# Optimization experiments

Hardware: AMD Instinct MI355X
Metric: run time of the kernel (lower is better)

Reference implementation:

```python
import jax, jax.numpy as jnp
import numpy as np

B, S_SRC, S_TGT, H, V = 32, 128, 64, 300, 32000


def setup_inputs() -> dict:
    key = jax.random.key(0)
    ks = jax.random.split(key, 16)

    def n(k, shape, scale=0.05):
        return jax.random.normal(k, shape, dtype=jnp.float32) * scale

    return {
        "x": jax.random.randint(ks[0], (B, S_SRC), 0, V),
        "y": jax.random.randint(ks[1], (B, S_TGT), 0, V),
        "h0": jax.random.normal(ks[2], (B, H), dtype=jnp.float32),  # encoder initNormState (L=1 squeezed)
        "EN": n(ks[3], (V, H)),
        "ZH": n(ks[4], (V, H)),
        "enc_Wih": n(ks[5], (H, H)),
        "enc_Whh": n(ks[6], (H, H)),
        "enc_bih": n(ks[7], (H,)),
        "enc_bhh": n(ks[8], (H,)),
        "dec_Wih": n(ks[9], (H, H)),
        "dec_Whh": n(ks[10], (H, H)),
        "dec_bih": n(ks[11], (H,)),
        "dec_bhh": n(ks[12], (H,)),
        "W_out": n(ks[13], (V, H)),
        "b_out": n(ks[14], (V,)),
    }


def reference(x, y, h0, EN, ZH, enc_Wih, enc_Whh, enc_bih, enc_bhh,
              dec_Wih, dec_Whh, dec_bih, dec_bhh, W_out, b_out):
    # ---- encoder: 1-layer tanh RNN over source embeddings ----
    xe = EN[x]  # [B, S_src, H]

    def enc_step(h, xt):  # xt: [B, H]
        h = jnp.tanh(xt @ enc_Wih.T + enc_bih + h @ enc_Whh.T + enc_bhh)
        return h, None

    c, _ = jax.lax.scan(enc_step, h0, jnp.swapaxes(xe, 0, 1))  # c: [B, H] final hidden

    # ---- decoder: original loop always feeds encoder state c (never the updated
    # hidden) to the RNNCell; with teacher forcing (start_TF_rate=1.0) every step
    # uses y_in[t], so all T steps vectorize into one batched computation. ----
    ye = ZH[y]  # [B, T, H]
    dec_state_term = c @ dec_Whh.T + dec_bhh  # [B, H], shared across all steps
    h_dec = jnp.tanh(ye @ dec_Wih.T + dec_bih + dec_state_term[:, None, :])  # [B, T, H]
    out = h_dec @ W_out.T + b_out  # [B, T, V]
    return out
```

## Files before the change

### kernel.cpp

```cpp
#include <hip/hip_runtime.h>
#include <hip/hip_bf16.h>
#include <stdint.h>

#define BB 32
#define S_SRC 128
#define S_TGT 64
#define H 300
#define VV 32000
#define M_ROWS (BB * S_TGT)
#define KP 320

#define MEGA_T 640
#define ENC_BLK 32
#define HDEC_BLK 128
#define WCVT_BLK 96

typedef __attribute__((ext_vector_type(8))) __bf16 bf16x8;
typedef __attribute__((ext_vector_type(4))) float f32x4;
typedef __attribute__((ext_vector_type(4))) unsigned short u16x4;
typedef __attribute__((ext_vector_type(2))) __fp16 f16x2;

#if defined(__has_builtin)
#if __has_builtin(__builtin_amdgcn_fdot2)
#define HAVE_FDOT2 1
#endif
#endif

__device__ inline unsigned short f2bf(float f) {
    union { float f; unsigned u; } v; v.f = f;
    unsigned r = (v.u + 0x7FFF + ((v.u >> 16) & 1)) >> 16;
    return (unsigned short)r;
}

__device__ __forceinline__ float ftanh(float x) {
    float e = __builtin_amdgcn_exp2f(x * 2.8853900817779268f);
    return 1.0f - 2.0f * __builtin_amdgcn_rcpf(e + 1.0f);
}

__device__ __forceinline__ float fdot2(f16x2 a, f16x2 b, float c) {
#ifdef HAVE_FDOT2
    return __builtin_amdgcn_fdot2(a, b, c, false);
#else
    return c + (float)a.x * (float)b.x + (float)a.y * (float)b.y;
#endif
}

__device__ __forceinline__ void gl_lds16(const void* g, void* l) {
    __builtin_amdgcn_global_load_lds(
        (const __attribute__((address_space(1))) void*)g,
        (__attribute__((address_space(3))) void*)l, 16, 0, 0);
}

__global__ void transpose2(const float* W0, const float* W1, float* dst) {
    const float* srcs[2] = {W0, W1};
    const float* src = srcs[blockIdx.z];
    float* d = dst + (size_t)blockIdx.z * (H * H);
    __shared__ float tile[32][33];
    int j0 = blockIdx.y * 32, k0 = blockIdx.x * 32;
    for (int r = threadIdx.y; r < 32; r += blockDim.y) {
        int j = j0 + r, k = k0 + threadIdx.x;
        tile[r][threadIdx.x] = (j < H && k < H) ? src[(size_t)j * H + k] : 0.f;
    }
    __syncthreads();
    for (int r = threadIdx.y; r < 32; r += blockDim.y) {
        int k = k0 + r, j = j0 + threadIdx.x;
        if (k < H && j < H) d[(size_t)k * H + j] = tile[threadIdx.x][r];
    }
}

#define RPB 8
__global__ __launch_bounds__(192) void pproj(const int* __restrict__ x,
                                             const float* __restrict__ EN,
                                             const float* __restrict__ WihT,
                                             const float* __restrict__ bih,
                                             const float* __restrict__ bhh,
                                             float* __restrict__ P) {
    __shared__ float xe[RPB][H];
    int m0 = blockIdx.x * RPB;
    int tid = threadIdx.x;
    for (int r = 0; r < RPB; ++r) {
        int idx = x[m0 + r];
        for (int c = tid; c < H; c += 192) xe[r][c] = EN[(size_t)idx * H + c];
    }
    __syncthreads();
    if (tid < 150) {
        int j = tid * 2;
        float a0[RPB], a1[RPB];
#pragma unroll
        for (int r = 0; r < RPB; ++r) { a0[r] = 0.f; a1[r] = 0.f; }
        const float* wp = WihT + j;
        for (int k = 0; k < H; ++k) {
            float2 w = *reinterpret_cast<const float2*>(wp + (size_t)k * H);
#pragma unroll
            for (int r = 0; r < RPB; ++r) {
                float xv = xe[r][k];
                a0[r] += xv * w.x; a1[r] += xv * w.y;
            }
        }
        float b0 = bih[j] + bhh[j], b1 = bih[j + 1] + bhh[j + 1];
#pragma unroll
        for (int r = 0; r < RPB; ++r) {
            P[(size_t)(m0 + r) * H + j]     = a0[r] + b0;
            P[(size_t)(m0 + r) * H + j + 1] = a1[r] + b1;
        }
    }
}

__global__ __launch_bounds__(MEGA_T) void mega(
    const float* __restrict__ h0, const float* __restrict__ P,
    const float* __restrict__ Whh,
    const float* __restrict__ dWhh, const float* __restrict__ dbhh,
    float* __restrict__ s2,
    const int* __restrict__ yv, const float* __restrict__ ZH,
    const float* __restrict__ WihT_d, const float* __restrict__ bih_d,
    float* __restrict__ t1,
    const float* __restrict__ W, unsigned short* __restrict__ Wb) {
    __shared__ union {
        __fp16 hb[2][304];
        float  ye[16][304];
    } L;
    int blk = blockIdx.x, tid = threadIdx.x;

    if (blk < ENC_BLK) {
        int b = blk;
        bool act = tid < 600;
        int j = tid >> 1, half = tid & 1;
        f16x2 w[76];
        if (act) {
            const float* wr = Whh + (size_t)j * H + half * 150;
#pragma unroll
            for (int i = 0; i < 75; ++i) {
                float2 f = *reinterpret_cast<const float2*>(wr + 2 * i);
                w[i] = __builtin_amdgcn_cvt_pkrtz(f.x, f.y);
            }
            w[75] = __builtin_amdgcn_cvt_pkrtz(0.f, 0.f);
        }
        if (act && half == 0) {
            int pos = j < 150 ? j : j + 2;
            L.hb[0][pos] = (__fp16)h0[(size_t)b * H + j];
        }
        if (tid >= 600 && tid < 608) {
            int pi = tid - 600, bufi = pi >> 2, q = pi & 3;
            int idx = (q < 2) ? (150 + q) : (302 + (q - 2));
            L.hb[bufi][idx] = (__fp16)0.f;
        }
        __syncthreads();

        const float* Pb = P + (size_t)b * S_SRC * H;
        int cur = 0;
        for (int t = 0; t < S_SRC; ++t) {
            float pv = 0.f;
            if (act && half == 0) pv = Pb[(size_t)t * H + j];
            if (act) {
                float a0 = 0.f, a1 = 0.f, a2 = 0.f, a3 = 0.f;
                const uint2* hp =
                    reinterpret_cast<const uint2*>(&L.hb[cur][half * 152]);
#pragma unroll
                for (int i = 0; i < 38; i += 2) {
                    uint2 qa = hp[i];
                    uint2 qb = hp[i + 1];
                    a0 = fdot2(w[2 * i],     __builtin_bit_cast(f16x2, qa.x), a0);
                    a1 = fdot2(w[2 * i + 1], __builtin_bit_cast(f16x2, qa.y), a1);
                    a2 = fdot2(w[2 * i + 2], __builtin_bit_cast(f16x2, qb.x), a2);
                    a3 = fdot2(w[2 * i + 3], __builtin_bit_cast(f16x2, qb.y), a3);
                }
                float a = (a0 + a1) + (a2 + a3);
                float tot = a + __shfl_xor(a, 1, 64);
                if (half == 0) {
                    float hv = ftanh(tot + pv);
                    int pos = j < 150 ? j : j + 2;
                    L.hb[cur ^ 1][pos] = (__fp16)hv;
                }
            }
            __syncthreads();
            cur ^= 1;
        }
        if (act) {
            const float* wr = dWhh + (size_t)j * H + half * 150;
            const uint2* hp = reinterpret_cast<const uint2*>(&L.hb[cur][half * 152]);
            float a0 = 0.f, a1 = 0.f;
#pragma unroll
            for (int i = 0; i < 37; ++i) {
                uint2 q = hp[i];
                f16x2 hA = __builtin_bit_cast(f16x2, q.x);
                f16x2 hB = __builtin_bit_cast(f16x2, q.y);
                float4 wf = *reinterpret_cast<const float4*>(wr + 4 * i);
                a0 += wf.x * (float)hA.x + wf.y * (float)hA.y;
                a1 += wf.z * (float)hB.x + wf.w * (float)hB.y;
            }
            {
                f16x2 hA = __builtin_bit_cast(f16x2,
                    reinterpret_cast<const uint*>(&L.hb[cur][half * 152])[74]);
                float2 wf = *reinterpret_cast<const float2*>(wr + 148);
                a0 += wf.x * (float)hA.x + wf.y * (float)hA.y;
            }
            float a = a0 + a1;
            float tot = a + __shfl_xor(a, 1, 64);
            if (half == 0) s2[(size_t)b * H + j] = tot + dbhh[j];
        }
    } else if (blk < ENC_BLK + HDEC_BLK) {
        int bi = blk - ENC_BLK;
        int m0 = bi * 16;
        for (int i = tid; i < 16 * 304; i += MEGA_T) {
            int r = i / 304, cc = i - r * 304;
            L.ye[r][cc] = (cc < H) ? ZH[(size_t)yv[m0 + r] * H + cc] : 0.f;
        }
        __syncthreads();
        if (tid < 600) {
            int rg = tid / 150, jp = tid - rg * 150, j0 = 2 * jp;
            float a[4][2] = {};
            const float* wp = WihT_d + j0;
            for (int k = 0; k < H; k += 2) {
                float2 wa = *reinterpret_cast<const float2*>(wp + (size_t)k * H);
                float2 wb = *reinterpret_cast<const float2*>(wp + (size_t)(k + 1) * H);
#pragma unroll
                for (int r = 0; r < 4; ++r) {
                    float2 x = *reinterpret_cast<const float2*>(&L.ye[rg * 4 + r][k]);
                    a[r][0] += x.x * wa.x + x.y * wb.x;
                    a[r][1] += x.x * wa.y + x.y * wb.y;
                }
            }
            float b0 = bih_d[j0], b1 = bih_d[j0 + 1];
#pragma unroll
            for (int r = 0; r < 4; ++r) {
                *reinterpret_cast<float2*>(&t1[(size_t)(m0 + rg * 4 + r) * 304 + j0]) =
                    make_float2(a[r][0] + b0, a[r][1] + b1);
            }
        }
    } else if (Wb != nullptr) {
        for (int id = (blk - (ENC_BLK + HDEC_BLK)) * MEGA_T + tid; id < VV * 80;
             id += WCVT_BLK * MEGA_T) {
            int row = id / 80, cq = id - row * 80;
            int k = cq * 4;
            u16x4 o;
            if (k < H) {
                float4 f = *reinterpret_cast<const float4*>(W + (size_t)row * H + k);
                o[0] = f2bf(f.x); o[1] = f2bf(f.y); o[2] = f2bf(f.z); o[3] = f2bf(f.w);
            } else {
                o[0] = 0; o[1] = 0; o[2] = 0; o[3] = 0;
            }
            *reinterpret_cast<u16x4*>(Wb + (size_t)row * KP + k) = o;
        }
    }
}

__global__ __launch_bounds__(256) void hdec_fin(const float* __restrict__ t1,
                                                const float* __restrict__ s2,
                                                unsigned short* __restrict__ hdec) {
    int blk = blockIdx.x, tid = threadIdx.x;
    for (int i = tid; i < 8 * KP; i += 256) {
        int r = i / KP, j = i - r * KP;
        int m = blk * 8 + r, b = m >> 6;
        unsigned short v = 0;
        if (j < H)
            v = f2bf(ftanh(t1[(size_t)m * 304 + j] + s2[(size_t)b * H + j]));
        hdec[(size_t)m * KP + j] = v;
    }
}

#define NBUF 4
__global__ __launch_bounds__(256, 2) void gemm4(const unsigned short* __restrict__ A,
                                                const unsigned short* __restrict__ Wb,
                                                const float* __restrict__ bout,
                                                float* __restrict__ out) {
    __shared__ unsigned short Al[NBUF][128 * 32];
    __shared__ unsigned short Bl[NBUF][128 * 32];
    int tid = threadIdx.x;
    int lane = tid & 63, wv = tid >> 6;
    int wm = wv >> 1, wn = wv & 1;

    int orig = blockIdx.x;
    int wg = (orig & 7) * 500 + (orig >> 3);
    int mi = wg & 15, ni = wg >> 4;
    int m0 = mi * 128, n0 = ni * 128;

    int rowq = tid >> 2;
    int scn = (tid & 3) ^ (rowq & 3);

    const unsigned short* Ab = A + (size_t)m0 * KP;
    const unsigned short* Bb = Wb + (size_t)n0 * KP;

    f32x4 acc[4][4];
    f32x4 zero = {0.f, 0.f, 0.f, 0.f};
#pragma unroll
    for (int i = 0; i < 4; ++i)
#pragma unroll
        for (int j = 0; j < 4; ++j) acc[i][j] = zero;

#define STAGE(T)                                                               \
    {                                                                          \
        int kk_ = (T) * 32;                                                    \
        int bf_ = (T) & 3;                                                     \
        _Pragma("unroll")                                                      \
        for (int s_ = 0; s_ < 2; ++s_) {                                       \
            int row_ = s_ * 64 + rowq;                                         \
            gl_lds16(Ab + (size_t)row_ * KP + kk_ + scn * 8,                   \
                     &Al[bf_][(s_ * 256 + tid) * 8]);                          \
        }                                                                      \
        _Pragma("unroll")                                                      \
        for (int s_ = 0; s_ < 2; ++s_) {                                       \
            int row_ = s_ * 64 + rowq;                                         \
            gl_lds16(Bb + (size_t)row_ * KP + kk_ + scn * 8,                   \
                     &Bl[bf_][(s_ * 256 + tid) * 8]);                          \
        }                                                                      \
    }

    STAGE(0) STAGE(1) STAGE(2)

#pragma unroll
    for (int t = 0; t < 10; ++t) {
        __builtin_amdgcn_sched_barrier(0);
        if (t < 8)       asm volatile("s_waitcnt vmcnt(8)" ::: "memory");
        else if (t == 8) asm volatile("s_waitcnt vmcnt(4)" ::: "memory");
        else             asm volatile("s_waitcnt vmcnt(0)" ::: "memory");
        __builtin_amdgcn_s_barrier();
        __builtin_amdgcn_sched_barrier(0);
        if (t + 3 < 10) STAGE(t + 3)
        int bf = t & 3;
        bf16x8 af[4], bb[4];
#pragma unroll
        for (int i = 0; i < 4; ++i) {
            int rowA = wm * 64 + i * 16 + (lane & 15);
            int chA = (lane >> 4) ^ (rowA & 3);
            af[i] = *reinterpret_cast<const bf16x8*>(&Al[bf][rowA * 32 + chA * 8]);
            int rowB = wn * 64 + i * 16 + (lane & 15);
            int chB = (lane >> 4) ^ (rowB & 3);
            bb[i] = *reinterpret_cast<const bf16x8*>(&Bl[bf][rowB * 32 + chB * 8]);
        }
        __builtin_amdgcn_s_setprio(1);
#pragma unroll
        for (int i = 0; i < 4; ++i)
#pragma unroll
            for (int j = 0; j < 4; ++j)
                acc[i][j] = __builtin_amdgcn_mfma_f32_16x16x32_bf16(
                    af[i], bb[j], acc[i][j], 0, 0, 0);
        __builtin_amdgcn_s_setprio(0);
    }
#undef STAGE

#pragma unroll
    for (int j = 0; j < 4; ++j) {
        int col = n0 + wn * 64 + j * 16 + (lane & 15);
        float bo = bout[col];
#pragma unroll
        for (int i = 0; i < 4; ++i) {
            int rb = m0 + wm * 64 + i * 16 + (lane >> 4) * 4;
            f32x4 v = acc[i][j];
#pragma unroll
            for (int r = 0; r < 4; ++r)
                out[(size_t)(rb + r) * VV + col] = v[r] + bo;
        }
    }
}

#define LDSW 40
__global__ __launch_bounds__(256) void gemm_out(const unsigned short* __restrict__ A,
                                                const float* __restrict__ W,
                                                const float* __restrict__ bout,
                                                float* __restrict__ out) {
    __shared__ __align__(16) unsigned short Alds[128 * LDSW];
    __shared__ __align__(16) unsigned short Bl[128 * LDSW];
    int tid = threadIdx.x;
    int lane = tid & 63, wv = tid >> 6;
    int wm = wv >> 1, wn = wv & 1;
    int m0 = blockIdx.y * 128, n0 = blockIdx.x * 128;

    f32x4 acc[4][4];
    f32x4 zero = {0.f, 0.f, 0.f, 0.f};
#pragma unroll
    for (int i = 0; i < 4; ++i)
#pragma unroll
        for (int jj = 0; jj < 4; ++jj) acc[i][jj] = zero;

    for (int k0 = 0; k0 < KP; k0 += 32) {
#pragma unroll
        for (int s = 0; s < 2; ++s) {
            int slot = tid + s * 256;
            int row = slot >> 2, c16 = slot & 3;
            uint4 v = *reinterpret_cast<const uint4*>(
                &A[(size_t)(m0 + row) * KP + k0 + c16 * 8]);
            *reinterpret_cast<uint4*>(&Alds[row * LDSW + c16 * 8]) = v;
        }
#pragma unroll
        for (int s = 0; s < 2; ++s) {
            int slot = tid + s * 256;
            int row = slot >> 2, c8 = slot & 3;
            int k = k0 + c8 * 8;
            __align__(16) unsigned short tmp[8];
            if (k + 7 < H) {
                const float* src = &W[(size_t)(n0 + row) * H + k];
                float4 f0 = *reinterpret_cast<const float4*>(src);
                float4 f1 = *reinterpret_cast<const float4*>(src + 4);
                tmp[0] = f2bf(f0.x); tmp[1] = f2bf(f0.y);
                tmp[2] = f2bf(f0.z); tmp[3] = f2bf(f0.w);
                tmp[4] = f2bf(f1.x); tmp[5] = f2bf(f1.y);
                tmp[6] = f2bf(f1.z); tmp[7] = f2bf(f1.w);
            } else {
#pragma unroll
                for (int jv = 0; jv < 8; ++jv) {
                    int kk = k + jv;
                    tmp[jv] = (kk < H) ? f2bf(W[(size_t)(n0 + row) * H + kk])
                                       : (unsigned short)0;
                }
            }
            *reinterpret_cast<uint4*>(&Bl[row * LDSW + c8 * 8]) =
                *reinterpret_cast<const uint4*>(tmp);
        }
        __syncthreads();
        bf16x8 af[4], bfm[4];
#pragma unroll
        for (int i = 0; i < 4; ++i) {
            int row = wm * 64 + i * 16 + (lane & 15);
            af[i] = *reinterpret_cast<const bf16x8*>(&Alds[row * LDSW + (lane >> 4) * 8]);
        }
#pragma unroll
        for (int i = 0; i < 4; ++i) {
            int row = wn * 64 + i * 16 + (lane & 15);
            bfm[i] = *reinterpret_cast<const bf16x8*>(&Bl[row * LDSW + (lane >> 4) * 8]);
        }
#pragma unroll
        for (int i = 0; i < 4; ++i)
#pragma unroll
            for (int jj = 0; jj < 4; ++jj)
                acc[i][jj] = __builtin_amdgcn_mfma_f32_16x16x32_bf16(
                    af[i], bfm[jj], acc[i][jj], 0, 0, 0);
        __syncthreads();
    }
#pragma unroll
    for (int jj = 0; jj < 4; ++jj) {
        int col = n0 + wn * 64 + jj * 16 + (lane & 15);
        float bo = bout[col];
#pragma unroll
        for (int i = 0; i < 4; ++i) {
            int rb = m0 + wm * 64 + i * 16 + (lane >> 4) * 4;
            f32x4 v = acc[i][jj];
#pragma unroll
            for (int r = 0; r < 4; ++r)
                out[(size_t)(rb + r) * VV + col] = v[r] + bo;
        }
    }
}

extern "C" void kernel_launch(void* const* d_in, const int* in_sizes, int n_in,
                              void* d_out, int out_size, void* d_ws, size_t ws_size,
                              hipStream_t stream) {
    const int*   x       = (const int*)d_in[0];
    const int*   y       = (const int*)d_in[1];
    const float* h0      = (const float*)d_in[2];
    const float* EN      = (const float*)d_in[3];
    const float* ZH      = (const float*)d_in[4];
    const float* enc_Wih = (const float*)d_in[5];
    const float* enc_Whh = (const float*)d_in[6];
    const float* enc_bih = (const float*)d_in[7];
    const float* enc_bhh = (const float*)d_in[8];
    const float* dec_Wih = (const float*)d_in[9];
    const float* dec_Whh = (const float*)d_in[10];
    const float* dec_bih = (const float*)d_in[11];
    const float* dec_bhh = (const float*)d_in[12];
    const float* W_out   = (const float*)d_in[13];
    const float* b_out   = (const float*)d_in[14];
    float* out = (float*)d_out;
    char* base = (char*)d_ws;

    const size_t needA = 22549120, needB = 2069120;
    bool bigws = (ws_size >= needA);
    if (!bigws && ws_size < needB) return;

    float* WT = (float*)base;
    float *s2_;
    unsigned short *hdec, *Wb = nullptr;
    if (bigws) {
        Wb   = (unsigned short*)(base + 720000);
        s2_  = (float*)(base + 21200000);
        hdec = (unsigned short*)(base + 21238400);
    } else {
        s2_  = (float*)(base + 720000);
        hdec = (unsigned short*)(base + 758400);
    }
    float* P  = out;
    float* t1 = out + 2000000;

    transpose2<<<dim3(10, 10, 2), dim3(32, 8), 0, stream>>>(enc_Wih, dec_Wih, WT);
    pproj<<<(BB * S_SRC) / RPB, 192, 0, stream>>>(x, EN, WT, enc_bih, enc_bhh, P);
    int mega_grid = bigws ? (ENC_BLK + HDEC_BLK + WCVT_BLK) : (ENC_BLK + HDEC_BLK);
    mega<<<mega_grid, MEGA_T, 0, stream>>>(h0, P, enc_Whh, dec_Whh, dec_bhh, s2_,
                                           y, ZH, WT + 90000, dec_bih, t1,
                                           W_out, Wb);
    hdec_fin<<<M_ROWS / 8, 256, 0, stream>>>(t1, s2_, hdec);
    if (bigws) {
        gemm4<<<4000, 256, 0, stream>>>(hdec, Wb, b_out, out);
    } else {
        gemm_out<<<dim3(VV / 128, M_ROWS / 128), 256, 0, stream>>>(hdec, W_out, b_out, out);
    }
}
```

Before: 263.5 us.

## Switch output GEMM to double-buffered higher-occupancy kernel; widen encoder input projection

The output-projection GEMM drops from a 4-stage LDS ring with hand-placed vmcnt waits and setprio to a simple 2-buffer scheme using __syncthreads. It requests 4 blocks per CU instead of 2 and uses a new XOR swizzle keyed on row pairs. The intent is to hide latency through occupancy rather than deep software pipelining, at the risk of exposing load latency per k-step. Separately, the encoder input projection now handles 16 rows per block and unrolls k by two with float2 LDS reads, to reuse each weight load across more rows.

```diff
diff --git a/kernel.cpp b/kernel.cpp
--- a/kernel.cpp
+++ b/kernel.cpp
@@ -68,7 +68,7 @@
     }
 }
 
-#define RPB 8
+#define RPB 16
 __global__ __launch_bounds__(192) void pproj(const int* __restrict__ x,
                                              const float* __restrict__ EN,
                                              const float* __restrict__ WihT,
@@ -89,12 +89,14 @@
 #pragma unroll
         for (int r = 0; r < RPB; ++r) { a0[r] = 0.f; a1[r] = 0.f; }
         const float* wp = WihT + j;
-        for (int k = 0; k < H; ++k) {
-            float2 w = *reinterpret_cast<const float2*>(wp + (size_t)k * H);
+        for (int k = 0; k < H; k += 2) {
+            float2 wa = *reinterpret_cast<const float2*>(wp + (size_t)k * H);
+            float2 wb = *reinterpret_cast<const float2*>(wp + (size_t)(k + 1) * H);
 #pragma unroll
             for (int r = 0; r < RPB; ++r) {
-                float xv = xe[r][k];
-                a0[r] += xv * w.x; a1[r] += xv * w.y;
+                float2 xv = *reinterpret_cast<const float2*>(&xe[r][k]);
+                a0[r] += xv.x * wa.x + xv.y * wb.x;
+                a1[r] += xv.x * wa.y + xv.y * wb.y;
             }
         }
         float b0 = bih[j] + bhh[j], b1 = bih[j + 1] + bhh[j + 1];
@@ -258,13 +260,12 @@
     }
 }
 
-#define NBUF 4
-__global__ __launch_bounds__(256, 2) void gemm4(const unsigned short* __restrict__ A,
+__global__ __launch_bounds__(256, 4) void gemm5(const unsigned short* __restrict__ A,
                                                 const unsigned short* __restrict__ Wb,
                                                 const float* __restrict__ bout,
                                                 float* __restrict__ out) {
-    __shared__ unsigned short Al[NBUF][128 * 32];
-    __shared__ unsigned short Bl[NBUF][128 * 32];
+    __shared__ unsigned short Al[2][128 * 32];
+    __shared__ unsigned short Bl[2][128 * 32];
     int tid = threadIdx.x;
     int lane = tid & 63, wv = tid >> 6;
     int wm = wv >> 1, wn = wv & 1;
@@ -275,7 +276,7 @@
     int m0 = mi * 128, n0 = ni * 128;
 
     int rowq = tid >> 2;
-    int scn = (tid & 3) ^ (rowq & 3);
+    int scn = (tid & 3) ^ ((rowq >> 1) & 3);
 
     const unsigned short* Ab = A + (size_t)m0 * KP;
     const unsigned short* Bb = Wb + (size_t)n0 * KP;
@@ -287,10 +288,10 @@
 #pragma unroll
         for (int j = 0; j < 4; ++j) acc[i][j] = zero;
 
-#define STAGE(T)                                                               \
+#define STAGE5(T)                                                              \
     {                                                                          \
         int kk_ = (T) * 32;                                                    \
-        int bf_ = (T) & 3;                                                     \
+        int bf_ = (T) & 1;                                                     \
         _Pragma("unroll")                                                      \
         for (int s_ = 0; s_ < 2; ++s_) {                                       \
             int row_ = s_ * 64 + rowq;                                         \
@@ -305,38 +306,30 @@
         }                                                                      \
     }
 
-    STAGE(0) STAGE(1) STAGE(2)
+    STAGE5(0)
 
 #pragma unroll
     for (int t = 0; t < 10; ++t) {
-        __builtin_amdgcn_sched_barrier(0);
-        if (t < 8)       asm volatile("s_waitcnt vmcnt(8)" ::: "memory");
-        else if (t == 8) asm volatile("s_waitcnt vmcnt(4)" ::: "memory");
-        else             asm volatile("s_waitcnt vmcnt(0)" ::: "memory");
-        __builtin_amdgcn_s_barrier();
-        __builtin_amdgcn_sched_barrier(0);
-        if (t + 3 < 10) STAGE(t + 3)
-        int bf = t & 3;
+        __syncthreads();
+        if (t < 9) STAGE5(t + 1)
+        int bf = t & 1;
+        int ch = (lane >> 4) ^ (((lane & 15) >> 1) & 3);
         bf16x8 af[4], bb[4];
 #pragma unroll
         for (int i = 0; i < 4; ++i) {
             int rowA = wm * 64 + i * 16 + (lane & 15);
-            int chA = (lane >> 4) ^ (rowA & 3);
-            af[i] = *reinterpret_cast<const bf16x8*>(&Al[bf][rowA * 32 + chA * 8]);
+            af[i] = *reinterpret_cast<const bf16x8*>(&Al[bf][rowA * 32 + ch * 8]);
             int rowB = wn * 64 + i * 16 + (lane & 15);
-            int chB = (lane >> 4) ^ (rowB & 3);
-            bb[i] = *reinterpret_cast<const bf16x8*>(&Bl[bf][rowB * 32 + chB * 8]);
-        }
-        __builtin_amdgcn_s_setprio(1);
+            bb[i] = *reinterpret_cast<const bf16x8*>(&Bl[bf][rowB * 32 + ch * 8]);
+        }
 #pragma unroll
         for (int i = 0; i < 4; ++i)
 #pragma unroll
             for (int j = 0; j < 4; ++j)
                 acc[i][j] = __builtin_amdgcn_mfma_f32_16x16x32_bf16(
                     af[i], bb[j], acc[i][j], 0, 0, 0);
-        __builtin_amdgcn_s_setprio(0);
-    }
-#undef STAGE
+    }
+#undef STAGE5
 
 #pragma unroll
     for (int j = 0; j < 4; ++j) {
@@ -488,7 +481,7 @@
                                            W_out, Wb);
     hdec_fin<<<M_ROWS / 8, 256, 0, stream>>>(t1, s2_, hdec);
     if (bigws) {
-        gemm4<<<4000, 256, 0, stream>>>(hdec, Wb, b_out, out);
+        gemm5<<<4000, 256, 0, stream>>>(hdec, Wb, b_out, out);
     } else {
         gemm_out<<<dim3(VV / 128, M_ROWS / 128), 256, 0, stream>>>(hdec, W_out, b_out, out);
     }
```

After: 318.0 us. 20.7% more time.
